# Optimization experiments

Hardware: AMD Instinct MI355X
Metric: run time of the kernel (lower is better)

Reference implementation:

```python
import jax, jax.numpy as jnp
import numpy as np

B, CIN, IMG = 2, 3, 128
E, NH, WS, L, HID = 256, 8, 8, 4, 1024
HD = E // NH
SCALE = HD ** -0.5
T = WS * WS  # tokens per window


def _layernorm(x, g, b):
    m = x.mean(-1, keepdims=True)
    v = ((x - m) ** 2).mean(-1, keepdims=True)
    return (x - m) * jax.lax.rsqrt(v + 1e-5) * g + b


def _build_mask(H, W, ws, ss):
    # Swin shifted-window mask, built with static numpy (H,W,ws,ss are static)
    img = np.zeros((H, W), np.float32)
    cnt = 0
    sl = lambda n: (slice(0, n - ws), slice(n - ws, n - ss), slice(n - ss, n))
    for h in sl(H):
        for w in sl(W):
            img[h, w] = cnt
            cnt += 1
    mw = img.reshape(H // ws, ws, W // ws, ws).transpose(0, 2, 1, 3).reshape(-1, ws * ws)
    d = mw[:, None, :] - mw[:, :, None]
    return jnp.asarray(np.where(d != 0, -100.0, 0.0).astype(np.float32))  # [nW,T,T]


def _win_attn(xseq, H, W, wqkv, bqkv, wproj, bproj, mask):
    Bn, N, C = xseq.shape
    nWh, nWw = H // WS, W // WS
    nW = nWh * nWw
    # window partition: [B,N,C] -> [B*nW, T, C]
    xw = xseq.reshape(Bn, nWh, WS, nWw, WS, C).transpose(0, 1, 3, 2, 4, 5).reshape(Bn * nW, T, C)
    qkv = (xw @ wqkv + bqkv).reshape(Bn * nW, T, 3, NH, HD).transpose(2, 0, 3, 1, 4)
    q, k, v = qkv[0], qkv[1], qkv[2]  # [B*nW, NH, T, HD]
    attn = jnp.einsum('whtd,whsd->whts', q, k) * SCALE
    if mask is not None:
        attn = (attn.reshape(Bn, nW, NH, T, T) + mask[None, :, None]).reshape(Bn * nW, NH, T, T)
    attn = jax.nn.softmax(attn, axis=-1)
    out = jnp.einsum('whts,whsd->wthd', attn, v).reshape(Bn * nW, T, C)
    out = out @ wproj + bproj
    # window merge
    out = out.reshape(Bn, nWh, nWw, WS, WS, C).transpose(0, 1, 3, 2, 4, 5).reshape(Bn, H * W, C)
    return out


def _forward(x, in_w, in_b, pos, ln1_g, ln1_b, qkv_w, qkv_b, proj_w, proj_b,
             ln2_g, ln2_b, mlp_w1, mlp_b1, mlp_w2, mlp_b2, out_w, out_b):
    Bx, _, H, W = x.shape
    ss = WS // 2
    y = jnp.einsum('bchw,ec->behw', x, in_w) + in_b[None, :, None, None] + pos
    seq = y.transpose(0, 2, 3, 1).reshape(Bx, H * W, E)
    mask = _build_mask(H, W, WS, ss)
    for i in range(L):
        shifted = (i % 2 == 1)
        if shifted:
            seq = jnp.roll(seq.reshape(Bx, H, W, E), (-ss, -ss), (1, 2)).reshape(Bx, H * W, E)
        h = _layernorm(seq, ln1_g[i], ln1_b[i])
        seq = seq + _win_attn(h, H, W, qkv_w[i], qkv_b[i], proj_w[i], proj_b[i],
                              mask if shifted else None)
        h = _layernorm(seq, ln2_g[i], ln2_b[i])
        seq = seq + (jax.nn.gelu(h @ mlp_w1[i] + mlp_b1[i], approximate=False) @ mlp_w2[i] + mlp_b2[i])
        if shifted:
            seq = jnp.roll(seq.reshape(Bx, H, W, E), (ss, ss), (1, 2)).reshape(Bx, H * W, E)
    out = seq.reshape(Bx, H, W, E).transpose(0, 3, 1, 2)
    return jnp.einsum('bchw,ec->behw', out, out_w) + out_b[None, :, None, None]


def setup_inputs() -> dict:
    key = jax.random.key(0)
    ks = jax.random.split(key, 10)
    std = jnp.float32(0.02)
    return {
        'x': jax.random.normal(ks[0], (B, CIN, IMG, IMG), jnp.float32),
        'in_w': jax.random.normal(ks[1], (E, CIN), jnp.float32) * std,
        'in_b': jnp.zeros((E,), jnp.float32),
        'pos': jax.random.normal(ks[2], (1, E, IMG, IMG), jnp.float32) * std,
        'ln1_g': jnp.ones((L, E), jnp.float32),
        'ln1_b': jnp.zeros((L, E), jnp.float32),
        'qkv_w': jax.random.normal(ks[3], (L, E, 3 * E), jnp.float32) * std,
        'qkv_b': jnp.zeros((L, 3 * E), jnp.float32),
        'proj_w': jax.random.normal(ks[4], (L, E, E), jnp.float32) * std,
        'proj_b': jnp.zeros((L, E), jnp.float32),
        'ln2_g': jnp.ones((L, E), jnp.float32),
        'ln2_b': jnp.zeros((L, E), jnp.float32),
        'mlp_w1': jax.random.normal(ks[5], (L, E, HID), jnp.float32) * std,
        'mlp_b1': jnp.zeros((L, HID), jnp.float32),
        'mlp_w2': jax.random.normal(ks[6], (L, HID, E), jnp.float32) * std,
        'mlp_b2': jnp.zeros((L, E), jnp.float32),
        'out_w': jax.random.normal(ks[7], (E, E), jnp.float32) * std,
        'out_b': jnp.zeros((E,), jnp.float32),
    }


def reference(x, in_w, in_b, pos, ln1_g, ln1_b, qkv_w, qkv_b, proj_w, proj_b,
              ln2_g, ln2_b, mlp_w1, mlp_b1, mlp_w2, mlp_b2, out_w, out_b):
    return _forward(x, in_w, in_b, pos, ln1_g, ln1_b, qkv_w, qkv_b, proj_w, proj_b,
                    ln2_g, ln2_b, mlp_w1, mlp_b1, mlp_w2, mlp_b2, out_w, out_b)
```

## Files before the change

### kernel.cpp

```cpp
#include <hip/hip_runtime.h>
#include <hip/hip_bf16.h>
#include <math.h>

#define E_DIM 256
#define NPB 16384
#define M_TOT 32768

typedef __attribute__((ext_vector_type(4))) float f32x4;
typedef __attribute__((ext_vector_type(8))) short s16x8;

__device__ inline unsigned short f2bu(float f) {
  __hip_bfloat16 h = __float2bfloat16(f);
  return *reinterpret_cast<unsigned short*>(&h);
}
__device__ inline float bu2f(unsigned short u) {
  union { unsigned int i; float f; } x; x.i = ((unsigned int)u) << 16; return x.f;
}
__device__ inline void gload16(const void* g, void* l) {
  __builtin_amdgcn_global_load_lds(
      (const __attribute__((address_space(1))) void*)g,
      (__attribute__((address_space(3))) void*)l, 16, 0, 0);
}
__device__ inline float fgelu(float v) {
  float u2 = 2.0f * v * (0.7978845608f + 0.0356774081f * v * v);
  u2 = fminf(u2, 30.0f);
  float e = __expf(u2);
  return v * (e / (e + 1.0f));
}

__global__ __launch_bounds__(256) void wconv_all(
    const float* __restrict__ qkv_w, const float* __restrict__ proj_w,
    const float* __restrict__ w1,    const float* __restrict__ w2,
    const float* __restrict__ outw,
    unsigned short* __restrict__ qkvT, unsigned short* __restrict__ projT,
    unsigned short* __restrict__ w1T,  unsigned short* __restrict__ w2T,
    unsigned short* __restrict__ outwb)
{
  int bid = blockIdx.x;
  if (bid >= 3072) {
    int idx = (bid - 3072) * 1024 + threadIdx.x * 4;
    float4 v = *(const float4*)(outw + idx);
    ushort4 u; u.x = f2bu(v.x); u.y = f2bu(v.y); u.z = f2bu(v.z); u.w = f2bu(v.w);
    *(ushort4*)(outwb + idx) = u;
    return;
  }
  int layer = bid / 768, r = bid % 768;
  const float* W; unsigned short* Wt; int K, N, txt, tile;
  if (r < 192)      { W = qkv_w  + (size_t)layer*196608; Wt = qkvT + (size_t)layer*196608; K=256;  N=768;  txt=24; tile=r; }
  else if (r < 256) { W = proj_w + (size_t)layer*65536;  Wt = projT+ (size_t)layer*65536;  K=256;  N=256;  txt=8;  tile=r-192; }
  else if (r < 512) { W = w1     + (size_t)layer*262144; Wt = w1T  + (size_t)layer*262144; K=256;  N=1024; txt=32; tile=r-256; }
  else              { W = w2     + (size_t)layer*262144; Wt = w2T  + (size_t)layer*262144; K=1024; N=256;  txt=8;  tile=r-512; }
  int nb = (tile % txt) * 32, kb = (tile / txt) * 32;
  __shared__ float t[32][33];
  int tx = threadIdx.x & 31, ty = threadIdx.x >> 5;
  #pragma unroll
  for (int i = 0; i < 32; i += 8)
    t[ty + i][tx] = W[(size_t)(kb + ty + i) * N + nb + tx];
  __syncthreads();
  #pragma unroll
  for (int i = 0; i < 32; i += 8)
    Wt[(size_t)(nb + ty + i) * K + kb + tx] = f2bu(t[tx][ty + i]);
}

__global__ __launch_bounds__(256) void embed_ln(
    const float* __restrict__ x, const float* __restrict__ in_w,
    const float* __restrict__ in_b, const float* __restrict__ pos,
    const float* __restrict__ g, const float* __restrict__ bta,
    float* __restrict__ seq, unsigned short* __restrict__ hb)
{
  __shared__ float ld[32][33];
  __shared__ float vbuf[32][260];
  __shared__ float2 st[32];
  const int n0 = blockIdx.x * 32;
  const int b = n0 >> 14, np = n0 & (NPB - 1);
  const int tx = threadIdx.x & 31, ty = threadIdx.x >> 5;

  float x0[4], x1[4], x2[4], sp[4] = {0,0,0,0}, qp[4] = {0,0,0,0};
  #pragma unroll
  for (int i = 0; i < 4; i++) {
    int n = np + ty + 8*i;
    x0[i] = x[(b*3 + 0)*NPB + n];
    x1[i] = x[(b*3 + 1)*NPB + n];
    x2[i] = x[(b*3 + 2)*NPB + n];
  }
  for (int ec = 0; ec < 8; ec++) {
    int e0 = ec * 32;
    #pragma unroll
    for (int i = 0; i < 4; i++)
      ld[ty + 8*i][tx] = pos[(size_t)(e0 + ty + 8*i) * NPB + np + tx];
    __syncthreads();
    #pragma unroll
    for (int i = 0; i < 4; i++) {
      int e = e0 + tx;
      float v = x0[i]*in_w[e*3+0] + x1[i]*in_w[e*3+1] + x2[i]*in_w[e*3+2]
              + in_b[e] + ld[tx][ty + 8*i];
      vbuf[ty + 8*i][e] = v;
      sp[i] += v; qp[i] += v * v;
    }
    __syncthreads();
  }
  #pragma unroll
  for (int i = 0; i < 4; i++) {
    #pragma unroll
    for (int off = 1; off < 32; off <<= 1) {
      sp[i] += __shfl_xor(sp[i], off);
      qp[i] += __shfl_xor(qp[i], off);
    }
    if (tx == 0) st[ty + 8*i] = (float2){sp[i], qp[i]};
  }
  __syncthreads();
  const int token = threadIdx.x >> 3, ch = threadIdx.x & 7;
  float2 sq = st[token];
  float mean = sq.x * (1.0f / 256.0f);
  float rstd = rsqrtf(sq.y * (1.0f / 256.0f) - mean * mean + 1e-5f);
  float* srow = seq + (size_t)(n0 + token) * 256;
  unsigned short* hrow = hb + (size_t)(n0 + token) * 256;
  #pragma unroll
  for (int u = 0; u < 8; u++) {
    int e = ch * 32 + u * 4;
    float4 v = *(float4*)&vbuf[token][e];
    *(float4*)(srow + e) = v;
    float4 gg = *(const float4*)(g + e);
    float4 bb = *(const float4*)(bta + e);
    ushort4 h;
    h.x = f2bu((v.x - mean) * rstd * gg.x + bb.x);
    h.y = f2bu((v.y - mean) * rstd * gg.y + bb.y);
    h.z = f2bu((v.z - mean) * rstd * gg.z + bb.z);
    h.w = f2bu((v.w - mean) * rstd * gg.w + bb.w);
    *(ushort4*)(hrow + e) = h;
  }
}

__device__ inline int rowf(int r) { return (r & 3) ^ ((r >> 2) & 3); }

template<int SHIFT>
__global__ __launch_bounds__(512) void qkv_attn(
    const unsigned short* __restrict__ hbuf, const unsigned short* __restrict__ qkvT,
    const float* __restrict__ qkv_b, unsigned short* __restrict__ hout)
{
  __shared__ unsigned short AQ[32768];
  __shared__ unsigned short Ks[16384];
  __shared__ unsigned short Vt[16384];
  const int tid = threadIdx.x, lane = tid & 63, wc = tid >> 6;
  const int lc = lane & 15, lg = lane >> 4;
  const int wf = blockIdx.x;
  const int b = wf >> 8, win = wf & 255;
  const int wh = win >> 4, ww = win & 15;

  auto tok_of = [&](int t) -> int {
    int hs = wh * 8 + (t >> 3), ws = ww * 8 + (t & 7);
    if (SHIFT) { hs = (hs + 4) & 127; ws = (ws + 4) & 127; }
    return b * NPB + hs * 128 + ws;
  };
  auto reg_of = [&](int t) -> int {
    int hs = wh * 8 + (t >> 3), ws = ww * 8 + (t & 7);
    int a = (hs < 120) ? 0 : ((hs < 124) ? 1 : 2);
    int c = (ws < 120) ? 0 : ((ws < 124) ? 1 : 2);
    return a * 3 + c;
  };

  #pragma unroll
  for (int jj = 0; jj < 4; jj++) {
    int chunk = tid + jj * 512;
    int r = chunk >> 5, c = chunk & 31;
    int cg = (c & 24) | ((c & 7) ^ (r & 7));
    gload16(hbuf + (size_t)tok_of(r) * 256 + cg * 8, (char*)AQ + chunk * 16);
  }
  __syncthreads();

  const int fmap0 = 2*wc, fmap1 = 2*wc+1, fmap2 = 16+2*wc, fmap3 = 17+2*wc,
            fmap4 = 32+2*wc, fmap5 = 33+2*wc;
  int fmap[6] = {fmap0, fmap1, fmap2, fmap3, fmap4, fmap5};
  f32x4 acc[4][6];
  #pragma unroll
  for (int m = 0; m < 4; m++)
    #pragma unroll
    for (int j = 0; j < 6; j++)
      acc[m][j] = (f32x4){0.f, 0.f, 0.f, 0.f};

  const unsigned short* bb[6];
  #pragma unroll
  for (int j = 0; j < 6; j++)
    bb[j] = qkvT + (size_t)(fmap[j] * 16 + lc) * 256 + lg * 8;

  s16x8 bcur[6];
  #pragma unroll
  for (int j = 0; j < 6; j++) bcur[j] = *(const s16x8*)(bb[j]);

  #pragma unroll
  for (int t = 0; t < 8; t++) {
    s16x8 bnext[6];
    if (t < 7) {
      #pragma unroll
      for (int j = 0; j < 6; j++) bnext[j] = *(const s16x8*)(bb[j] + (t + 1) * 32);
    }
    s16x8 aF[4];
    #pragma unroll
    for (int m = 0; m < 4; m++) {
      int r = m * 16 + lc;
      int g = t * 4 + lg;
      int cc = (g & 24) | ((g & 7) ^ (r & 7));
      aF[m] = *(const s16x8*)(AQ + r * 256 + cc * 8);
    }
    #pragma unroll
    for (int m = 0; m < 4; m++)
      #pragma unroll
      for (int j = 0; j < 6; j++)
        acc[m][j] = __builtin_amdgcn_mfma_f32_16x16x32_bf16(aF[m], bcur[j], acc[m][j], 0, 0, 0);
    if (t < 7) {
      #pragma unroll
      for (int j = 0; j < 6; j++) bcur[j] = bnext[j];
    }
  }

  float bv[6];
  #pragma unroll
  for (int j = 0; j < 6; j++) bv[j] = qkv_b[fmap[j] * 16 + lc];
  const float scale = 0.17677669529663687f;

  #pragma unroll
  for (int j = 0; j < 6; j++) {
    int col = fmap[j] * 16 + lc;
    #pragma unroll
    for (int m = 0; m < 4; m++)
      #pragma unroll
      for (int r = 0; r < 4; r++) {
        int t = m * 16 + lg * 4 + r;
        float v = acc[m][j][r] + bv[j];
        if (j < 2) {
          int qc = col, c = qc >> 3;
          int cc = (c & 24) | ((c & 7) ^ (t & 7));
          AQ[16384 + t * 256 + cc * 8 + (qc & 7)] = f2bu(v * scale);
        } else if (j < 4) {
          int kc = col - 256, c = kc >> 3;
          int cc = (c & 24) | ((c & 7) ^ (t & 7));
          Ks[t * 256 + cc * 8 + (kc & 7)] = f2bu(v);
        } else {
          int d = col - 512 - wc * 32;
          int tc = (t >> 3) ^ (d & 7);
          Vt[wc * 2048 + d * 64 + tc * 8 + (t & 7)] = f2bu(v);
        }
      }
  }

  s16x8 qf[4], kf[4];
  #pragma unroll
  for (int m = 0; m < 4; m++) {
    int t = m * 16 + lc;
    int g = wc * 4 + lg;
    int cc = (g & 24) | ((g & 7) ^ (t & 7));
    qf[m] = *(const s16x8*)(AQ + 16384 + t * 256 + cc * 8);
    kf[m] = *(const s16x8*)(Ks + t * 256 + cc * 8);
  }
  __syncthreads();

  f32x4 sT[4][4];
  #pragma unroll
  for (int m = 0; m < 4; m++)
    #pragma unroll
    for (int qt = 0; qt < 4; qt++) {
      f32x4 z = (f32x4){0.f, 0.f, 0.f, 0.f};
      sT[m][qt] = __builtin_amdgcn_mfma_f32_16x16x32_bf16(kf[m], qf[qt], z, 0, 0, 0);
    }

  int qreg[4], kreg2[16];
  if (SHIFT) {
    #pragma unroll
    for (int qt = 0; qt < 4; qt++) qreg[qt] = reg_of(qt * 16 + lc);
    #pragma unroll
    for (int m = 0; m < 4; m++)
      #pragma unroll
      for (int r = 0; r < 4; r++) kreg2[m * 4 + r] = reg_of(m * 16 + lg * 4 + r);
  }

  unsigned short* Pl = AQ + wc * 4096;
  #pragma unroll
  for (int qt = 0; qt < 4; qt++) {
    float mx = -1e30f;
    #pragma unroll
    for (int m = 0; m < 4; m++)
      #pragma unroll
      for (int r = 0; r < 4; r++) {
        float s = sT[m][qt][r];
        if (SHIFT && qreg[qt] != kreg2[m * 4 + r]) s -= 100.0f;
        sT[m][qt][r] = s;
        mx = fmaxf(mx, s);
      }
    mx = fmaxf(mx, __shfl_xor(mx, 16));
    mx = fmaxf(mx, __shfl_xor(mx, 32));
    float sum = 0.f;
    #pragma unroll
    for (int m = 0; m < 4; m++)
      #pragma unroll
      for (int r = 0; r < 4; r++) {
        float p = __expf(sT[m][qt][r] - mx);
        sT[m][qt][r] = p;
        sum += p;
      }
    sum += __shfl_xor(sum, 16);
    sum += __shfl_xor(sum, 32);
    float inv = 1.0f / sum;
    int q = qt * 16 + lc;
    #pragma unroll
    for (int m = 0; m < 4; m++) {
      ushort4 pk;
      pk.x = f2bu(sT[m][qt][0] * inv);
      pk.y = f2bu(sT[m][qt][1] * inv);
      pk.z = f2bu(sT[m][qt][2] * inv);
      pk.w = f2bu(sT[m][qt][3] * inv);
      *(ushort4*)(Pl + ((q * 64 + m * 16 + lg * 4) ^ ((q & 7) << 3))) = pk;
    }
  }

  f32x4 oacc[4][2];
  #pragma unroll
  for (int qt = 0; qt < 4; qt++)
    #pragma unroll
    for (int n = 0; n < 2; n++)
      oacc[qt][n] = (f32x4){0.f, 0.f, 0.f, 0.f};
  #pragma unroll
  for (int kb = 0; kb < 2; kb++) {
    s16x8 pa[4], vb[2];
    #pragma unroll
    for (int qt = 0; qt < 4; qt++) {
      int q = qt * 16 + lc;
      pa[qt] = *(const s16x8*)(Pl + ((q * 64 + kb * 32 + lg * 8) ^ ((q & 7) << 3)));
    }
    #pragma unroll
    for (int n = 0; n < 2; n++) {
      int d = n * 16 + lc;
      vb[n] = *(const s16x8*)(Vt + wc * 2048 + d * 64 + (((kb * 4 + lg) ^ (d & 7)) * 8));
    }
    #pragma unroll
    for (int qt = 0; qt < 4; qt++)
      #pragma unroll
      for (int n = 0; n < 2; n++)
        oacc[qt][n] = __builtin_amdgcn_mfma_f32_16x16x32_bf16(pa[qt], vb[n], oacc[qt][n], 0, 0, 0);
  }

  #pragma unroll
  for (int qt = 0; qt < 4; qt++)
    #pragma unroll
    for (int r = 0; r < 4; r++) {
      int q = qt * 16 + lg * 4 + r;
      unsigned short* ob = hout + (size_t)tok_of(q) * 256 + wc * 32;
      ob[lc]      = f2bu(oacc[qt][0][r]);
      ob[16 + lc] = f2bu(oacc[qt][1][r]);
    }
}

template<int ACT, int OCHW, int OBF>
__global__ __launch_bounds__(512) void mgemm_a(
    const unsigned short* __restrict__ A, const unsigned short* __restrict__ Wt,
    const float* __restrict__ bias, void* __restrict__ Cv, int N, int K)
{
  __shared__ unsigned short Al[2][128 * 32];
  __shared__ unsigned short Bl[2][256 * 32];
  const int tid  = threadIdx.x;
  const int lane = tid & 63;
  const int wid  = tid >> 6;
  const int wr = wid >> 2, wc = wid & 3;
  const int nbx = N >> 8;
  const int bid = blockIdx.x;
  const int lt  = (bid & 7) * ((int)gridDim.x >> 3) + (bid >> 3);
  const int bn  = (lt % nbx) * 256, bm = (lt / nbx) * 128;

  f32x4 acc[4][4];
  #pragma unroll
  for (int m = 0; m < 4; m++)
    #pragma unroll
    for (int n = 0; n < 4; n++)
      acc[m][n] = (f32x4){0.f, 0.f, 0.f, 0.f};

  const int srow = tid >> 2;
  const int cs   = (tid & 3) ^ rowf(srow);
  const unsigned short* aSrc  = A  + (size_t)(bm + srow) * K + cs * 8;
  const unsigned short* bSrc0 = Wt + (size_t)(bn + srow) * K + cs * 8;
  const unsigned short* bSrc1 = Wt + (size_t)(bn + srow + 128) * K + cs * 8;

  const int slotx = (lane >> 4) ^ (lane & 3) ^ ((lane >> 2) & 3);
  const int aoff = (wr*64 + (lane & 15)) * 64 + slotx * 16;
  const int boff = (wc*64 + (lane & 15)) * 64 + slotx * 16;

  {
    gload16(aSrc,  (char*)Al[0] + tid * 16);
    gload16(bSrc0, (char*)Bl[0] + tid * 16);
    gload16(bSrc1, (char*)Bl[0] + tid * 16 + 8192);
  }
  __syncthreads();

  const int nt = K >> 5;
  int cur = 0;
  for (int t = 0; t < nt; ++t) {
    if (t + 1 < nt) {
      int k0 = (t + 1) << 5;
      gload16(aSrc + k0,  (char*)Al[cur ^ 1] + tid * 16);
      gload16(bSrc0 + k0, (char*)Bl[cur ^ 1] + tid * 16);
      gload16(bSrc1 + k0, (char*)Bl[cur ^ 1] + tid * 16 + 8192);
    }
    const char* ab = (const char*)Al[cur] + aoff;
    const char* bbp = (const char*)Bl[cur] + boff;
    s16x8 af[4], bf_[4];
    #pragma unroll
    for (int m = 0; m < 4; m++) af[m]  = *(const s16x8*)(ab + m * 1024);
    #pragma unroll
    for (int n = 0; n < 4; n++) bf_[n] = *(const s16x8*)(bbp + n * 1024);
    #pragma unroll
    for (int m = 0; m < 4; m++)
      #pragma unroll
      for (int n = 0; n < 4; n++)
        acc[m][n] = __builtin_amdgcn_mfma_f32_16x16x32_bf16(af[m], bf_[n], acc[m][n], 0, 0, 0);
    __syncthreads();
    cur ^= 1;
  }

  float bv[4];
  #pragma unroll
  for (int n = 0; n < 4; n++) bv[n] = bias[bn + wc*64 + n*16 + (lane & 15)];

  #pragma unroll
  for (int m = 0; m < 4; m++) {
    int row0 = bm + wr*64 + m*16 + (lane >> 4) * 4;
    #pragma unroll
    for (int n = 0; n < 4; n++) {
      int col = bn + wc*64 + n*16 + (lane & 15);
      if (OCHW) {
        int bb2 = row0 >> 14, n0 = row0 & (NPB - 1);
        float4 st;
        st.x = acc[m][n][0] + bv[n]; st.y = acc[m][n][1] + bv[n];
        st.z = acc[m][n][2] + bv[n]; st.w = acc[m][n][3] + bv[n];
        *(float4*)((float*)Cv + (size_t)bb2 * E_DIM * NPB + (size_t)col * NPB + n0) = st;
      } else {
        #pragma unroll
        for (int j = 0; j < 4; j++) {
          int row = row0 + j;
          float v = acc[m][n][j] + bv[n];
          if (ACT) v = fgelu(v);
          if (OBF) ((unsigned short*)Cv)[(size_t)row * N + col] = f2bu(v);
          else     ((float*)Cv)[(size_t)row * N + col] = v;
        }
      }
    }
  }
}

template<int LNC>
__global__ __launch_bounds__(512) void mgemm_res(
    const unsigned short* __restrict__ A, const unsigned short* __restrict__ Wt,
    const float* __restrict__ bias, float* __restrict__ seq,
    const float* __restrict__ gamma, const float* __restrict__ beta,
    unsigned short* __restrict__ hb, int K)
{
  __shared__ unsigned short Al[2][64 * 32];
  __shared__ unsigned short Bl[2][256 * 32];
  __shared__ float2 ws[64][4];
  const int tid  = threadIdx.x;
  const int lane = tid & 63;
  const int wid  = tid >> 6;
  const int wr = wid >> 2, wc = wid & 3;
  const int bid = blockIdx.x;
  const int lt  = (bid & 7) * ((int)gridDim.x >> 3) + (bid >> 3);
  const int bm  = lt * 64;

  f32x4 acc[2][4];
  #pragma unroll
  for (int m = 0; m < 2; m++)
    #pragma unroll
    for (int n = 0; n < 4; n++)
      acc[m][n] = (f32x4){0.f, 0.f, 0.f, 0.f};

  const int srow = tid >> 2;
  const int cs   = (tid & 3) ^ rowf(srow);
  const unsigned short* aSrc  = A  + (size_t)(bm + srow) * K + cs * 8;
  const unsigned short* bSrc0 = Wt + (size_t)srow * K + cs * 8;
  const unsigned short* bSrc1 = Wt + (size_t)(srow + 128) * K + cs * 8;

  const int slotx = (lane >> 4) ^ (lane & 3) ^ ((lane >> 2) & 3);
  const int aoff = (wr*32 + (lane & 15)) * 64 + slotx * 16;
  const int boff = (wc*64 + (lane & 15)) * 64 + slotx * 16;

  {
    if (tid < 256) gload16(aSrc, (char*)Al[0] + tid * 16);
    gload16(bSrc0, (char*)Bl[0] + tid * 16);
    gload16(bSrc1, (char*)Bl[0] + tid * 16 + 8192);
  }
  __syncthreads();

  const int nt = K >> 5;
  int cur = 0;
  for (int t = 0; t < nt; ++t) {
    if (t + 1 < nt) {
      int k0 = (t + 1) << 5;
      if (tid < 256) gload16(aSrc + k0, (char*)Al[cur ^ 1] + tid * 16);
      gload16(bSrc0 + k0, (char*)Bl[cur ^ 1] + tid * 16);
      gload16(bSrc1 + k0, (char*)Bl[cur ^ 1] + tid * 16 + 8192);
    }
    const char* ab = (const char*)Al[cur] + aoff;
    const char* bbp = (const char*)Bl[cur] + boff;
    s16x8 af[2], bf_[4];
    #pragma unroll
    for (int m = 0; m < 2; m++) af[m]  = *(const s16x8*)(ab + m * 1024);
    #pragma unroll
    for (int n = 0; n < 4; n++) bf_[n] = *(const s16x8*)(bbp + n * 1024);
    #pragma unroll
    for (int m = 0; m < 2; m++)
      #pragma unroll
      for (int n = 0; n < 4; n++)
        acc[m][n] = __builtin_amdgcn_mfma_f32_16x16x32_bf16(af[m], bf_[n], acc[m][n], 0, 0, 0);
    __syncthreads();
    cur ^= 1;
  }

  const int lc = lane & 15, lg = lane >> 4;
  float bv[4], gv[4], btv[4];
  #pragma unroll
  for (int n = 0; n < 4; n++) {
    int col = wc*64 + n*16 + lc;
    bv[n] = bias[col];
    if (LNC) { gv[n] = gamma[col]; btv[n] = beta[col]; }
  }

  #pragma unroll
  for (int m = 0; m < 2; m++)
    #pragma unroll
    for (int j = 0; j < 4; j++) {
      int row = bm + wr*32 + m*16 + lg*4 + j;
      #pragma unroll
      for (int n = 0; n < 4; n++) {
        int col = wc*64 + n*16 + lc;
        float v = acc[m][n][j] + bv[n] + seq[(size_t)row * 256 + col];
        seq[(size_t)row * 256 + col] = v;
        acc[m][n][j] = v;
      }
    }

  if (LNC) {
    #pragma unroll
    for (int m = 0; m < 2; m++)
      #pragma unroll
      for (int j = 0; j < 4; j++) {
        float s = acc[m][0][j] + acc[m][1][j] + acc[m][2][j] + acc[m][3][j];
        float q = acc[m][0][j]*acc[m][0][j] + acc[m][1][j]*acc[m][1][j]
                + acc[m][2][j]*acc[m][2][j] + acc[m][3][j]*acc[m][3][j];
        s += __shfl_xor(s, 1); q += __shfl_xor(q, 1);
        s += __shfl_xor(s, 2); q += __shfl_xor(q, 2);
        s += __shfl_xor(s, 4); q += __shfl_xor(q, 4);
        s += __shfl_xor(s, 8); q += __shfl_xor(q, 8);
        if (lc == 0) ws[wr*32 + m*16 + lg*4 + j][wc] = (float2){s, q};
      }
    __syncthreads();
  }

  #pragma unroll
  for (int m = 0; m < 2; m++)
    #pragma unroll
    for (int j = 0; j < 4; j++) {
      int r = wr*32 + m*16 + lg*4 + j;
      float mean = 0.f, rstd = 1.f;
      if (LNC) {
        float2 a0 = ws[r][0], a1 = ws[r][1], a2 = ws[r][2], a3 = ws[r][3];
        float s = a0.x + a1.x + a2.x + a3.x;
        float q = a0.y + a1.y + a2.y + a3.y;
        mean = s * (1.0f / 256.0f);
        rstd = rsqrtf(q * (1.0f / 256.0f) - mean * mean + 1e-5f);
      }
      unsigned short* hrow = hb + (size_t)(bm + r) * 256;
      #pragma unroll
      for (int n = 0; n < 4; n++) {
        int col = wc*64 + n*16 + lc;
        float o = LNC ? (acc[m][n][j] - mean) * rstd * gv[n] + btv[n]
                      : acc[m][n][j];
        hrow[col] = f2bu(o);
      }
    }
}

extern "C" void kernel_launch(void* const* d_in, const int* in_sizes, int n_in,
                              void* d_out, int out_size, void* d_ws, size_t ws_size,
                              hipStream_t stream) {
  (void)in_sizes; (void)n_in; (void)out_size; (void)ws_size;
  const float* x      = (const float*)d_in[0];
  const float* in_w   = (const float*)d_in[1];
  const float* in_b   = (const float*)d_in[2];
  const float* pos    = (const float*)d_in[3];
  const float* ln1_g  = (const float*)d_in[4];
  const float* ln1_b  = (const float*)d_in[5];
  const float* qkv_w  = (const float*)d_in[6];
  const float* qkv_b  = (const float*)d_in[7];
  const float* proj_w = (const float*)d_in[8];
  const float* proj_b = (const float*)d_in[9];
  const float* ln2_g  = (const float*)d_in[10];
  const float* ln2_b  = (const float*)d_in[11];
  const float* mlp_w1 = (const float*)d_in[12];
  const float* mlp_b1 = (const float*)d_in[13];
  const float* mlp_w2 = (const float*)d_in[14];
  const float* mlp_b2 = (const float*)d_in[15];
  const float* out_w  = (const float*)d_in[16];
  const float* out_b  = (const float*)d_in[17];
  float* outp = (float*)d_out;

  char* p = (char*)d_ws;
  float* seq = (float*)p;                 p += (size_t)M_TOT * E_DIM * 4;
  unsigned short* bigb = (unsigned short*)p; p += (size_t)M_TOT * 1024 * 2;
  unsigned short* hb = (unsigned short*)p;   p += (size_t)M_TOT * E_DIM * 2;
  unsigned short* wb = (unsigned short*)p;
  unsigned short* qkvT = wb;
  unsigned short* projT = qkvT + 4 * 768 * 256;
  unsigned short* w1T   = projT + 4 * 256 * 256;
  unsigned short* w2T   = w1T   + 4 * 1024 * 256;
  unsigned short* outwb = w2T   + 4 * 256 * 1024;

  wconv_all<<<3136, 256, 0, stream>>>(qkv_w, proj_w, mlp_w1, mlp_w2, out_w,
                                      qkvT, projT, w1T, w2T, outwb);
  embed_ln<<<1024, 256, 0, stream>>>(x, in_w, in_b, pos, ln1_g, ln1_b, seq, hb);

  for (int i = 0; i < 4; i++) {
    int shifted = i & 1;
    if (shifted) qkv_attn<1><<<512, 512, 0, stream>>>(hb, qkvT + (size_t)i*768*256, qkv_b + i*768, hb);
    else         qkv_attn<0><<<512, 512, 0, stream>>>(hb, qkvT + (size_t)i*768*256, qkv_b + i*768, hb);
    mgemm_res<1><<<512, 512, 0, stream>>>(
        hb, projT + (size_t)i*256*256, proj_b + i*256, seq,
        ln2_g + i*256, ln2_b + i*256, hb, 256);
    mgemm_a<1,0,1><<<1024, 512, 0, stream>>>(
        hb, w1T + (size_t)i*1024*256, mlp_b1 + i*1024, bigb, 1024, 256);
    if (i < 3)
      mgemm_res<1><<<512, 512, 0, stream>>>(
          bigb, w2T + (size_t)i*256*1024, mlp_b2 + i*256, seq,
          ln1_g + (i+1)*256, ln1_b + (i+1)*256, hb, 1024);
    else
      mgemm_res<0><<<512, 512, 0, stream>>>(
          bigb, w2T + (size_t)i*256*1024, mlp_b2 + i*256, seq,
          nullptr, nullptr, hb, 1024);
  }

  mgemm_a<0,1,0><<<256, 512, 0, stream>>>(
      hb, outwb, out_b, outp, 256, 256);
}
```

Before: 606.3 us.

## Fuse MLP up-projection, GELU and down-projection into one kernel

```diff
diff --git a/kernel.cpp b/kernel.cpp
--- a/kernel.cpp
+++ b/kernel.cpp
@@ -320,7 +320,7 @@
       oacc[qt][n] = (f32x4){0.f, 0.f, 0.f, 0.f};
   #pragma unroll
   for (int kb = 0; kb < 2; kb++) {
-    s16x8 pa[4], vb[2];
+    s16x8 pa[4], vb2[2];
     #pragma unroll
     for (int qt = 0; qt < 4; qt++) {
       int q = qt * 16 + lc;
@@ -329,13 +329,13 @@
     #pragma unroll
     for (int n = 0; n < 2; n++) {
       int d = n * 16 + lc;
-      vb[n] = *(const s16x8*)(Vt + wc * 2048 + d * 64 + (((kb * 4 + lg) ^ (d & 7)) * 8));
+      vb2[n] = *(const s16x8*)(Vt + wc * 2048 + d * 64 + (((kb * 4 + lg) ^ (d & 7)) * 8));
     }
     #pragma unroll
     for (int qt = 0; qt < 4; qt++)
       #pragma unroll
       for (int n = 0; n < 2; n++)
-        oacc[qt][n] = __builtin_amdgcn_mfma_f32_16x16x32_bf16(pa[qt], vb[n], oacc[qt][n], 0, 0, 0);
+        oacc[qt][n] = __builtin_amdgcn_mfma_f32_16x16x32_bf16(pa[qt], vb2[n], oacc[qt][n], 0, 0, 0);
   }
 
   #pragma unroll
@@ -346,6 +346,165 @@
       unsigned short* ob = hout + (size_t)tok_of(q) * 256 + wc * 32;
       ob[lc]      = f2bu(oacc[qt][0][r]);
       ob[16 + lc] = f2bu(oacc[qt][1][r]);
+    }
+}
+
+template<int LNC>
+__global__ __launch_bounds__(512, 2) void fused_mlp(
+    const unsigned short* __restrict__ A, const unsigned short* __restrict__ w1T,
+    const unsigned short* __restrict__ w2T,
+    const float* __restrict__ b1, const float* __restrict__ b2,
+    float* __restrict__ seq,
+    const float* __restrict__ gamma, const float* __restrict__ beta,
+    unsigned short* __restrict__ hb)
+{
+  __shared__ unsigned short Ast[16384];
+  __shared__ unsigned short Hid[65536];
+  const int tid = threadIdx.x, lane = tid & 63, wc = tid >> 6;
+  const int lc = lane & 15, lg = lane >> 4;
+  const int bid = blockIdx.x;
+  const int lt = (bid & 7) * ((int)gridDim.x >> 3) + (bid >> 3);
+  const int bm = lt * 64;
+
+  #pragma unroll
+  for (int jj = 0; jj < 4; jj++) {
+    int chunk = tid + jj * 512;
+    int r = chunk >> 5, c = chunk & 31;
+    int cg = (c & 24) | ((c & 7) ^ (r & 7));
+    gload16(A + (size_t)(bm + r) * 256 + cg * 8, (char*)Ast + chunk * 16);
+  }
+  __syncthreads();
+
+  {
+    f32x4 acc[4][8];
+    #pragma unroll
+    for (int m = 0; m < 4; m++)
+      #pragma unroll
+      for (int n = 0; n < 8; n++)
+        acc[m][n] = (f32x4){0.f, 0.f, 0.f, 0.f};
+    #pragma unroll
+    for (int t = 0; t < 8; t++) {
+      s16x8 aF[4];
+      #pragma unroll
+      for (int m = 0; m < 4; m++) {
+        int r = m * 16 + lc;
+        int g = t * 4 + lg;
+        int cc = (g & 24) | ((g & 7) ^ (r & 7));
+        aF[m] = *(const s16x8*)(Ast + r * 256 + cc * 8);
+      }
+      s16x8 bF[8];
+      #pragma unroll
+      for (int n = 0; n < 8; n++)
+        bF[n] = *(const s16x8*)(w1T + (size_t)(wc * 128 + n * 16 + lc) * 256 + t * 32 + lg * 8);
+      #pragma unroll
+      for (int m = 0; m < 4; m++)
+        #pragma unroll
+        for (int n = 0; n < 8; n++)
+          acc[m][n] = __builtin_amdgcn_mfma_f32_16x16x32_bf16(aF[m], bF[n], acc[m][n], 0, 0, 0);
+    }
+    float bias1[8];
+    #pragma unroll
+    for (int n = 0; n < 8; n++) bias1[n] = b1[wc * 128 + n * 16 + lc];
+    #pragma unroll
+    for (int m = 0; m < 4; m++)
+      #pragma unroll
+      for (int n = 0; n < 8; n++)
+        #pragma unroll
+        for (int r = 0; r < 4; r++) {
+          int row = m * 16 + lg * 4 + r;
+          int k = wc * 128 + n * 16 + lc;
+          float v = fgelu(acc[m][n][r] + bias1[n]);
+          int c = k >> 3;
+          int cc = (c & 120) | ((c & 7) ^ (row & 7));
+          Hid[row * 1024 + cc * 8 + (k & 7)] = f2bu(v);
+        }
+  }
+  __syncthreads();
+
+  f32x4 acc2[4][2];
+  #pragma unroll
+  for (int m = 0; m < 4; m++)
+    #pragma unroll
+    for (int n = 0; n < 2; n++)
+      acc2[m][n] = (f32x4){0.f, 0.f, 0.f, 0.f};
+  for (int kk = 0; kk < 32; kk++) {
+    s16x8 aF[4];
+    #pragma unroll
+    for (int m = 0; m < 4; m++) {
+      int row = m * 16 + lc;
+      int c = kk * 4 + lg;
+      int cc = (c & 120) | ((c & 7) ^ (row & 7));
+      aF[m] = *(const s16x8*)(Hid + row * 1024 + cc * 8);
+    }
+    s16x8 bF[2];
+    #pragma unroll
+    for (int n = 0; n < 2; n++)
+      bF[n] = *(const s16x8*)(w2T + (size_t)(wc * 32 + n * 16 + lc) * 1024 + kk * 32 + lg * 8);
+    #pragma unroll
+    for (int m = 0; m < 4; m++)
+      #pragma unroll
+      for (int n = 0; n < 2; n++)
+        acc2[m][n] = __builtin_amdgcn_mfma_f32_16x16x32_bf16(aF[m], bF[n], acc2[m][n], 0, 0, 0);
+  }
+
+  float bv[2], gv[2], btv[2];
+  #pragma unroll
+  for (int n = 0; n < 2; n++) {
+    int col = wc * 32 + n * 16 + lc;
+    bv[n] = b2[col];
+    if (LNC) { gv[n] = gamma[col]; btv[n] = beta[col]; }
+  }
+  #pragma unroll
+  for (int m = 0; m < 4; m++)
+    #pragma unroll
+    for (int j = 0; j < 4; j++) {
+      int row = bm + m * 16 + lg * 4 + j;
+      #pragma unroll
+      for (int n = 0; n < 2; n++) {
+        int col = wc * 32 + n * 16 + lc;
+        float v = acc2[m][n][j] + bv[n] + seq[(size_t)row * 256 + col];
+        seq[(size_t)row * 256 + col] = v;
+        acc2[m][n][j] = v;
+      }
+    }
+
+  float2* ws = (float2*)Ast;
+  if (LNC) {
+    #pragma unroll
+    for (int m = 0; m < 4; m++)
+      #pragma unroll
+      for (int j = 0; j < 4; j++) {
+        float s = acc2[m][0][j] + acc2[m][1][j];
+        float q = acc2[m][0][j]*acc2[m][0][j] + acc2[m][1][j]*acc2[m][1][j];
+        s += __shfl_xor(s, 1); q += __shfl_xor(q, 1);
+        s += __shfl_xor(s, 2); q += __shfl_xor(q, 2);
+        s += __shfl_xor(s, 4); q += __shfl_xor(q, 4);
+        s += __shfl_xor(s, 8); q += __shfl_xor(q, 8);
+        if (lc == 0) ws[(m * 16 + lg * 4 + j) * 8 + wc] = (float2){s, q};
+      }
+    __syncthreads();
+  }
+  #pragma unroll
+  for (int m = 0; m < 4; m++)
+    #pragma unroll
+    for (int j = 0; j < 4; j++) {
+      int r = m * 16 + lg * 4 + j;
+      float mean = 0.f, rstd = 1.f;
+      if (LNC) {
+        float s = 0.f, q = 0.f;
+        #pragma unroll
+        for (int w = 0; w < 8; w++) { float2 a = ws[r * 8 + w]; s += a.x; q += a.y; }
+        mean = s * (1.0f / 256.0f);
+        rstd = rsqrtf(q * (1.0f / 256.0f) - mean * mean + 1e-5f);
+      }
+      unsigned short* hrow = hb + (size_t)(bm + r) * 256;
+      #pragma unroll
+      for (int n = 0; n < 2; n++) {
+        int col = wc * 32 + n * 16 + lc;
+        float o = LNC ? (acc2[m][n][j] - mean) * rstd * gv[n] + btv[n]
+                      : acc2[m][n][j];
+        hrow[col] = f2bu(o);
+      }
     }
 }
 
@@ -609,6 +768,7 @@
   unsigned short* w1T   = projT + 4 * 256 * 256;
   unsigned short* w2T   = w1T   + 4 * 1024 * 256;
   unsigned short* outwb = w2T   + 4 * 256 * 1024;
+  (void)bigb;
 
   wconv_all<<<3136, 256, 0, stream>>>(qkv_w, proj_w, mlp_w1, mlp_w2, out_w,
                                       qkvT, projT, w1T, w2T, outwb);
@@ -621,16 +781,16 @@
     mgemm_res<1><<<512, 512, 0, stream>>>(
         hb, projT + (size_t)i*256*256, proj_b + i*256, seq,
         ln2_g + i*256, ln2_b + i*256, hb, 256);
-    mgemm_a<1,0,1><<<1024, 512, 0, stream>>>(
-        hb, w1T + (size_t)i*1024*256, mlp_b1 + i*1024, bigb, 1024, 256);
     if (i < 3)
-      mgemm_res<1><<<512, 512, 0, stream>>>(
-          bigb, w2T + (size_t)i*256*1024, mlp_b2 + i*256, seq,
-          ln1_g + (i+1)*256, ln1_b + (i+1)*256, hb, 1024);
+      fused_mlp<1><<<512, 512, 0, stream>>>(
+          hb, w1T + (size_t)i*1024*256, w2T + (size_t)i*256*1024,
+          mlp_b1 + i*1024, mlp_b2 + i*256, seq,
+          ln1_g + (i+1)*256, ln1_b + (i+1)*256, hb);
     else
-      mgemm_res<0><<<512, 512, 0, stream>>>(
-          bigb, w2T + (size_t)i*256*1024, mlp_b2 + i*256, seq,
-          nullptr, nullptr, hb, 1024);
+      fused_mlp<0><<<512, 512, 0, stream>>>(
+          hb, w1T + (size_t)i*1024*256, w2T + (size_t)i*256*1024,
+          mlp_b1 + i*1024, mlp_b2 + i*256, seq,
+          nullptr, nullptr, hb);
   }
 
   mgemm_a<0,1,0><<<256, 512, 0, stream>>>(
```

Result: slower. 716.7 us (+18.2%).
